# Kernel tuning notes

Measured on AMD Instinct MI355X. Metric: run time of the kernel, lower is better.

Reference implementation:

```python
import jax, jax.numpy as jnp
import numpy as np

NAT, NN = 10000, 32
RSN, THETAN, NEMB = 16, 8, 4
RC = 5.0
ZETA = 16.0
FEAT = RSN * NEMB + RSN * THETAN * NEMB  # 576
PI = 3.141592653589793


def setup_inputs() -> dict:
    key = jax.random.key(0)
    ks = jax.random.split(key, 12)
    positions = jax.random.normal(ks[0], (NAT, 3), dtype=jnp.float32) * 2.0
    species_encoder = jax.random.normal(ks[1], (NAT, NEMB), dtype=jnp.float32)
    theta_s = jax.random.uniform(ks[2], (THETAN,), dtype=jnp.float32) * PI
    kn_rad = jnp.ones((1,), dtype=jnp.float32)
    neighbor_idx = jax.random.randint(ks[3], (NAT, NN), 0, NAT, dtype=jnp.int32)
    W1 = jax.random.normal(ks[4], (FEAT, 64), dtype=jnp.float32) / np.sqrt(FEAT)
    b1 = jnp.zeros((64,), dtype=jnp.float32)
    W2 = jax.random.normal(ks[5], (64, 64), dtype=jnp.float32) / 8.0
    b2 = jnp.zeros((64,), dtype=jnp.float32)
    W3 = jax.random.normal(ks[6], (64, 1), dtype=jnp.float32) / 8.0
    b3 = jnp.zeros((1,), dtype=jnp.float32)
    return {"positions": positions, "species_encoder": species_encoder,
            "theta_s": theta_s, "kn_rad": kn_rad,
            "W1": W1, "b1": b1, "W2": W2, "b2": b2, "W3": W3, "b3": b3,
            "neighbor_idx": neighbor_idx}


def _bessel_radial(rnorm, kn_rad):
    # spherical-Bessel radial basis with smooth cosine cutoff (help_fn.bessel_function)
    fc = 0.5 * (jnp.cos(PI * rnorm / RC) + 1.0) * (rnorm < RC).astype(rnorm.dtype)
    k = jnp.arange(1, RSN + 1, dtype=rnorm.dtype)                     # [RSN]
    arg = (PI / RC) * kn_rad[0] * k[None, None, :] * rnorm[..., None]  # [nat,NN,RSN]
    return jnp.sqrt(2.0 / RC) * jnp.sin(arg) / rnorm[..., None] * fc[..., None]


def reference(positions, species_encoder, theta_s, kn_rad,
              W1, b1, W2, b2, W3, b3, neighbor_idx):
    # gather neighbor displacements: [nat, NN, 3]
    rij = positions[neighbor_idx] - positions[:, None, :]
    rnorm = jnp.linalg.norm(rij, axis=-1) + 1e-8                      # [nat, NN]

    bf = _bessel_radial(rnorm, kn_rad)                                # [nat, NN, RSN]
    # center-x-neighbor species embedding product (einsum 'ijk->ik->ijk')
    semb_ij = species_encoder[neighbor_idx] * species_encoder[:, None, :]  # [nat,NN,NEMB]

    # radial descriptors: [nat, RSN, NEMB] -> [nat, RSN*NEMB]
    desc_rad = jnp.einsum('ijl,ijm->ilm', bf, semb_ij).reshape(NAT, -1)

    # angular part
    rij_unit = rij / rnorm[..., None]
    cos_ijk = jnp.einsum('ijc,ikc->ijk', rij_unit, rij_unit)          # [nat,NN,NN]
    cos_ijk = jnp.clip(cos_ijk, -1.0 + 1e-6, 1.0 - 1e-6)
    sin_ijk = jnp.sqrt(1.0 - cos_ijk * cos_ijk)
    ct, st = jnp.cos(theta_s), jnp.sin(theta_s)

    # factorized per-bond channel tensor P: [nat, NN, RSN*NEMB]
    P = jnp.einsum('ijl,ijm->ijlm', bf, semb_ij).reshape(NAT, NN, RSN * NEMB)
    pref = 2.0 ** (1.0 - ZETA)
    ang = []
    for t in range(THETAN):  # small fixed loop over angle centers
        cosd = cos_ijk * ct[t] + sin_ijk * st[t]                      # cos(theta - theta_s)
        A = pref * (1.0 + cosd) ** ZETA                               # [nat,NN,NN]
        C = jnp.einsum('ijk,ijp->ikp', A, P)                          # contract over j
        ang.append(jnp.sum(C * P, axis=1))                            # [nat, RSN*NEMB]
    desc_ang = jnp.stack(ang, axis=1).reshape(NAT, -1)                # [nat, THETAN*RSN*NEMB]

    desc = jnp.concatenate([desc_rad, desc_ang], axis=1)              # [nat, FEAT]

    # per-atom MLP -> atomic energies, scatter-sum to total energy
    h = jnp.tanh(desc @ W1 + b1)
    h = jnp.tanh(h @ W2 + b2)
    e_atom = (h @ W3 + b3)[:, 0]                                      # [nat]
    return jnp.sum(e_atom)
```

## Files before the change

### kernel.cpp

```cpp
#include <hip/hip_runtime.h>
#include <hip/hip_bf16.h>

#define NATC 10000
#define NATP 10016
#define NNC 32
#define RSNC 16
#define THETANC 8
#define NEMBC 4
#define FEATC 576

typedef __attribute__((ext_vector_type(8))) short short8;
typedef __attribute__((ext_vector_type(4))) float f32x4;
typedef __attribute__((ext_vector_type(2))) float f32x2;

static __device__ __forceinline__ short f2bf(float x) {
    union { __hip_bfloat16 h; short s; } u;
    u.h = __float2bfloat16(x);
    return u.s;
}

__global__ __launch_bounds__(256) void prep_kernel(
    const float* __restrict__ W1, const float* __restrict__ W2,
    const float* __restrict__ b3,
    ushort* __restrict__ W1p, ushort* __restrict__ W2p,
    float* __restrict__ out)
{
    const int gid = blockIdx.x * 256 + threadIdx.x;
    if (gid == 0) out[0] = (float)NATC * b3[0];
    if (gid < 4608) {
        const int l = gid & 63, ntks = gid >> 6;
        const int nt = ntks & 3, ks = ntks >> 2;
        const int q = l >> 4, c = l & 15;
        ushort pk[8];
        #pragma unroll
        for (int jj = 0; jj < 8; ++jj)
            pk[jj] = (ushort)f2bf(W1[(ks * 32 + q * 8 + jj) * 64 + nt * 16 + c]);
        #pragma unroll
        for (int jj = 0; jj < 8; ++jj) W1p[gid * 8 + jj] = pk[jj];
    } else {
        const int g = gid - 4608;
        const int l = g & 63, ntks = g >> 6;
        const int nt = ntks & 3, ks = ntks >> 2;
        const int q = l >> 4, c = l & 15;
        ushort pk[8];
        #pragma unroll
        for (int jj = 0; jj < 8; ++jj)
            pk[jj] = (ushort)f2bf(W2[(ks * 32 + q * 8 + jj) * 64 + nt * 16 + c]);
        #pragma unroll
        for (int jj = 0; jj < 8; ++jj) W2p[g * 8 + jj] = pk[jj];
    }
}

__global__ __launch_bounds__(256, 7) void desc_kernel(
    const float* __restrict__ pos,
    const float* __restrict__ spe,
    const float* __restrict__ theta_s,
    const float* __restrict__ kn_rad,
    const int* __restrict__ nidx,
    ushort* __restrict__ descb)
{
    constexpr float RC = 5.0f;
    constexpr float PI_F = 3.14159265358979323846f;
    constexpr float SF = 0.52213689121f;

    __shared__ f32x4 Pt4[64 * 9];
    __shared__ f32x4 cs4[32 * 17];
    __shared__ float thc[16];
    __shared__ __attribute__((aligned(16))) char uni[4096];

    float* const Pt    = (float*)Pt4;
    float* const ux    = (float*)uni;
    float* const uy    = ux + 32;
    float* const uz    = ux + 64;
    float* const rbase = ux + 96;
    float* const rw    = ux + 128;
    float* const bfs   = ux + 160;
    float* const ses   = ux + 704;
    short* const Pb    = (short*)uni;

    const int i   = blockIdx.x;
    const int tid = threadIdx.x;

    if (tid < NNC) {
        const int j = tid;
        const int n = nidx[i * NNC + j];
        const float pix = pos[i * 3 + 0], piy = pos[i * 3 + 1], piz = pos[i * 3 + 2];
        const float dx = pos[n * 3 + 0] - pix;
        const float dy = pos[n * 3 + 1] - piy;
        const float dz = pos[n * 3 + 2] - piz;
        const float r = sqrtf(dx * dx + dy * dy + dz * dz) + 1e-8f;
        const float inv = 1.0f / r;
        ux[j] = dx * inv; uy[j] = dy * inv; uz[j] = dz * inv;
        const float fc = (r < RC) ? 0.5f * (cosf(PI_F * r * (1.0f / RC)) + 1.0f) : 0.0f;
        rbase[j] = sqrtf(2.0f / RC) * inv * fc;
        rw[j]    = (PI_F / RC) * kn_rad[0] * r;
        #pragma unroll
        for (int m = 0; m < NEMBC; ++m)
            ses[j * 5 + m] = spe[n * NEMBC + m] * spe[i * NEMBC + m];
    } else if (tid >= 64 && tid < 72) {
        const int t = tid - 64;
        const float th = theta_s[t];
        thc[2 * t]     = SF * cosf(th);
        thc[2 * t + 1] = SF * sinf(th);
    }
    __syncthreads();

    #pragma unroll
    for (int k = 0; k < 2; ++k) {
        const int e = tid + k * 256;
        const int j = e >> 4, l = e & 15;
        bfs[j * 17 + l] = rbase[j] * sinf(rw[j] * (float)(l + 1));
    }
    __syncthreads();

    #pragma unroll
    for (int k = 0; k < 8; ++k) {
        const int e = tid + k * 256;
        const int j = e & 31, p = e >> 5;
        Pt[p * 36 + j] = bfs[j * 17 + (p >> 2)] * ses[j * 5 + (p & 3)];
    }
    #pragma unroll
    for (int k = 0; k < 4; ++k) {
        const int e = tid + k * 256;
        const int kk = e & 31, j = e >> 5;
        float cv = ux[j] * ux[kk] + uy[j] * uy[kk] + uz[j] * uz[kk];
        cv = fminf(fmaxf(cv, -1.0f + 1e-6f), 1.0f - 1e-6f);
        f32x2 csv;
        csv[0] = cv;
        csv[1] = sqrtf(fmaxf(1.0f - cv * cv, 0.0f));
        ((f32x2*)cs4)[kk * 34 + j] = csv;
    }
    __syncthreads();

    {
        const int nt = tid >> 6, l2 = tid & 63;
        const int q2 = l2 >> 4, c2 = l2 & 15;
        const f32x4 x0 = Pt4[(nt * 16 + c2) * 9 + q2 * 2];
        const f32x4 x1 = Pt4[(nt * 16 + c2) * 9 + q2 * 2 + 1];
        short8 pk;
        pk[0] = f2bf(x0[0]); pk[1] = f2bf(x0[1]); pk[2] = f2bf(x0[2]); pk[3] = f2bf(x0[3]);
        pk[4] = f2bf(x1[0]); pk[5] = f2bf(x1[1]); pk[6] = f2bf(x1[2]); pk[7] = f2bf(x1[3]);
        *(short8*)&Pb[tid * 8] = pk;
    }
    if (tid < 64) {
        const f32x4* pr = &Pt4[tid * 9];
        float s = 0.0f;
        #pragma unroll
        for (int kb = 0; kb < 8; ++kb) {
            const f32x4 v = pr[kb];
            s += v[0]; s += v[1]; s += v[2]; s += v[3];
        }
        descb[(size_t)i * FEATC + tid] = (ushort)f2bf(s);
    }
    __syncthreads();

    const int w = tid >> 6, l = tid & 63;
    const int q = l >> 4, c = l & 15;

    #pragma unroll
    for (int tt = 0; tt < 2; ++tt) {
        const int t = w + tt * 4;
        const float tc = thc[2 * t], ts = thc[2 * t + 1];

        short8 afr[2];
        #pragma unroll
        for (int mt = 0; mt < 2; ++mt) {
            const int kk = mt * 16 + c;
            const f32x4* crow = &cs4[kk * 17 + q * 4];
            const f32x4 vv[4] = { crow[0], crow[1], crow[2], crow[3] };
            #pragma unroll
            for (int jj = 0; jj < 8; ++jj) {
                const float cv = vv[jj >> 1][(jj & 1) * 2];
                const float sv = vv[jj >> 1][(jj & 1) * 2 + 1];
                const float y  = fmaf(cv, tc, fmaf(sv, ts, SF));
                const float y2 = y * y, y4 = y2 * y2, y8 = y4 * y4;
                afr[mt][jj] = f2bf(y8 * y8);
            }
        }

        f32x4 acc[2][4];
        #pragma unroll
        for (int mt = 0; mt < 2; ++mt)
            #pragma unroll
            for (int nt = 0; nt < 4; ++nt)
                acc[mt][nt] = (f32x4){0.0f, 0.0f, 0.0f, 0.0f};

        #pragma unroll
        for (int nt = 0; nt < 4; ++nt) {
            const short8 bfr = *(const short8*)&Pb[(nt * 64 + l) * 8];
            acc[0][nt] = __builtin_amdgcn_mfma_f32_16x16x32_bf16(afr[0], bfr, acc[0][nt], 0, 0, 0);
            acc[1][nt] = __builtin_amdgcn_mfma_f32_16x16x32_bf16(afr[1], bfr, acc[1][nt], 0, 0, 0);
        }

        float ptv[4];
        #pragma unroll
        for (int nt = 0; nt < 4; ++nt) {
            float s = 0.0f;
            #pragma unroll
            for (int mt = 0; mt < 2; ++mt) {
                const f32x4 pv = Pt4[(nt * 16 + c) * 9 + mt * 4 + q];
                #pragma unroll
                for (int r = 0; r < 4; ++r)
                    s = fmaf(acc[mt][nt][r], pv[r], s);
            }
            s += __shfl_xor(s, 16, 64);
            s += __shfl_xor(s, 32, 64);
            ptv[nt] = s;
        }
        const float v = (q == 0) ? ptv[0] : (q == 1) ? ptv[1] : (q == 2) ? ptv[2] : ptv[3];
        descb[(size_t)i * FEATC + 64 + t * 64 + l] = (ushort)f2bf(v);
    }
}

__global__ __launch_bounds__(256) void mlp_kernel(
    const ushort* __restrict__ descb,
    const ushort* __restrict__ W1p, const float* __restrict__ b1,
    const ushort* __restrict__ W2p, const float* __restrict__ b2,
    const float* __restrict__ W3,
    float* __restrict__ out)
{
    __shared__ __attribute__((aligned(16))) ushort H1b[16 * 72];
    __shared__ float red[4];

    const int tid = threadIdx.x;
    const int w = tid >> 6, l = tid & 63;
    const int q = l >> 4, c = l & 15;
    const int a0 = blockIdx.x * 16;

    f32x4 acc = (f32x4){0.0f, 0.0f, 0.0f, 0.0f};

    #pragma unroll 6
    for (int ks = 0; ks < 18; ++ks) {
        const short8 b   = *(const short8*)&W1p[((ks * 4 + w) * 64 + l) * 8];
        const short8 afr = *(const short8*)&descb[(size_t)(a0 + c) * FEATC + ks * 32 + q * 8];
        acc = __builtin_amdgcn_mfma_f32_16x16x32_bf16(afr, b, acc, 0, 0, 0);
    }

    const float b1v = b1[w * 16 + c];
    #pragma unroll
    for (int r = 0; r < 4; ++r)
        H1b[(q * 4 + r) * 72 + w * 16 + c] = (ushort)f2bf(tanhf(acc[r] + b1v));
    __syncthreads();

    f32x4 acc2 = (f32x4){0.0f, 0.0f, 0.0f, 0.0f};
    #pragma unroll
    for (int ks = 0; ks < 2; ++ks) {
        const short8 b   = *(const short8*)&W2p[((ks * 4 + w) * 64 + l) * 8];
        const short8 afr = *(const short8*)&H1b[c * 72 + ks * 32 + q * 8];
        acc2 = __builtin_amdgcn_mfma_f32_16x16x32_bf16(afr, b, acc2, 0, 0, 0);
    }

    const float b2v = b2[w * 16 + c];
    const float w3v = W3[w * 16 + c];
    float s = 0.0f;
    #pragma unroll
    for (int r = 0; r < 4; ++r) {
        const int a = a0 + q * 4 + r;
        if (a < NATC) s += tanhf(acc2[r] + b2v) * w3v;
    }
    #pragma unroll
    for (int off = 1; off <= 32; off <<= 1)
        s += __shfl_xor(s, off, 64);
    if (l == 0) red[w] = s;
    __syncthreads();
    if (tid == 0)
        atomicAdd(out, red[0] + red[1] + red[2] + red[3]);
}

extern "C" void kernel_launch(void* const* d_in, const int* in_sizes, int n_in,
                              void* d_out, int out_size, void* d_ws, size_t ws_size,
                              hipStream_t stream)
{
    const float* pos   = (const float*)d_in[0];
    const float* spe   = (const float*)d_in[1];
    const float* theta = (const float*)d_in[2];
    const float* kn    = (const float*)d_in[3];
    const float* W1    = (const float*)d_in[4];
    const float* b1    = (const float*)d_in[5];
    const float* W2    = (const float*)d_in[6];
    const float* b2    = (const float*)d_in[7];
    const float* W3    = (const float*)d_in[8];
    const float* b3    = (const float*)d_in[9];
    const int*   nidx  = (const int*)d_in[10];
    float* out = (float*)d_out;

    ushort* descb = (ushort*)d_ws;
    ushort* W1p   = (ushort*)((char*)d_ws + (size_t)NATP * FEATC * 2);
    ushort* W2p   = W1p + 4608 * 8;

    prep_kernel<<<20, 256, 0, stream>>>(W1, W2, b3, W1p, W2p, out);
    desc_kernel<<<NATC, 256, 0, stream>>>(pos, spe, theta, kn, nidx, descb);
    mlp_kernel<<<(NATC + 15) / 16, 256, 0, stream>>>(descb, W1p, b1, W2p, b2, W3, out);
}
```

Baseline: 134.4 us.

## Merge prep into desc kernel, use sin recurrence and packed FP32 math

New measurement: 132.3 us. About the same (-1.5%).

```diff
diff --git a/kernel.cpp b/kernel.cpp
--- a/kernel.cpp
+++ b/kernel.cpp
@@ -19,67 +19,87 @@
     return u.s;
 }
 
-__global__ __launch_bounds__(256) void prep_kernel(
+static __device__ __forceinline__ f32x2 pk_fma(f32x2 a, f32x2 b, f32x2 c) {
+    f32x2 d;
+    asm("v_pk_fma_f32 %0, %1, %2, %3" : "=v"(d) : "v"(a), "v"(b), "v"(c));
+    return d;
+}
+static __device__ __forceinline__ f32x2 pk_mul(f32x2 a, f32x2 b) {
+    f32x2 d;
+    asm("v_pk_mul_f32 %0, %1, %2" : "=v"(d) : "v"(a), "v"(b));
+    return d;
+}
+static __device__ __forceinline__ int cvt_pk_bf16(float lo, float hi) {
+    int r;
+    asm("v_cvt_pk_bf16_f32 %0, %1, %2" : "=v"(r) : "v"(lo), "v"(hi));
+    return r;
+}
+
+static __device__ __forceinline__ int pow16_pair(f32x2 cv, f32x2 sv,
+                                                 f32x2 tcv, f32x2 tsv, f32x2 sfv) {
+    f32x2 y = pk_fma(cv, tcv, pk_fma(sv, tsv, sfv));
+    y = pk_mul(y, y);
+    y = pk_mul(y, y);
+    y = pk_mul(y, y);
+    y = pk_mul(y, y);
+    return cvt_pk_bf16(y[0], y[1]);
+}
+
+__global__ __launch_bounds__(256, 5) void desc_kernel(
+    const float* __restrict__ pos,
+    const float* __restrict__ spe,
+    const float* __restrict__ theta_s,
+    const float* __restrict__ kn_rad,
+    const int* __restrict__ nidx,
+    ushort* __restrict__ descb,
     const float* __restrict__ W1, const float* __restrict__ W2,
     const float* __restrict__ b3,
     ushort* __restrict__ W1p, ushort* __restrict__ W2p,
     float* __restrict__ out)
 {
-    const int gid = blockIdx.x * 256 + threadIdx.x;
-    if (gid == 0) out[0] = (float)NATC * b3[0];
-    if (gid < 4608) {
-        const int l = gid & 63, ntks = gid >> 6;
-        const int nt = ntks & 3, ks = ntks >> 2;
-        const int q = l >> 4, c = l & 15;
-        ushort pk[8];
-        #pragma unroll
-        for (int jj = 0; jj < 8; ++jj)
-            pk[jj] = (ushort)f2bf(W1[(ks * 32 + q * 8 + jj) * 64 + nt * 16 + c]);
-        #pragma unroll
-        for (int jj = 0; jj < 8; ++jj) W1p[gid * 8 + jj] = pk[jj];
-    } else {
-        const int g = gid - 4608;
-        const int l = g & 63, ntks = g >> 6;
-        const int nt = ntks & 3, ks = ntks >> 2;
-        const int q = l >> 4, c = l & 15;
-        ushort pk[8];
-        #pragma unroll
-        for (int jj = 0; jj < 8; ++jj)
-            pk[jj] = (ushort)f2bf(W2[(ks * 32 + q * 8 + jj) * 64 + nt * 16 + c]);
-        #pragma unroll
-        for (int jj = 0; jj < 8; ++jj) W2p[g * 8 + jj] = pk[jj];
-    }
-}
-
-__global__ __launch_bounds__(256, 7) void desc_kernel(
-    const float* __restrict__ pos,
-    const float* __restrict__ spe,
-    const float* __restrict__ theta_s,
-    const float* __restrict__ kn_rad,
-    const int* __restrict__ nidx,
-    ushort* __restrict__ descb)
-{
     constexpr float RC = 5.0f;
     constexpr float PI_F = 3.14159265358979323846f;
     constexpr float SF = 0.52213689121f;
 
-    __shared__ f32x4 Pt4[64 * 9];
-    __shared__ f32x4 cs4[32 * 17];
+    const int tid = threadIdx.x;
+
+    if (blockIdx.x >= NATC) {
+        const int gid = (blockIdx.x - NATC) * 256 + tid;
+        if (gid == 0) out[0] = (float)NATC * b3[0];
+        if (gid < 4608) {
+            const int l = gid & 63, ntks = gid >> 6;
+            const int nt = ntks & 3, ks = ntks >> 2;
+            const int qq = l >> 4, cc = l & 15;
+            ushort pk[8];
+            #pragma unroll
+            for (int jj = 0; jj < 8; ++jj)
+                pk[jj] = (ushort)f2bf(W1[(ks * 32 + qq * 8 + jj) * 64 + nt * 16 + cc]);
+            #pragma unroll
+            for (int jj = 0; jj < 8; ++jj) W1p[gid * 8 + jj] = pk[jj];
+        } else {
+            const int g = gid - 4608;
+            const int l = g & 63, ntks = g >> 6;
+            const int nt = ntks & 3, ks = ntks >> 2;
+            const int qq = l >> 4, cc = l & 15;
+            ushort pk[8];
+            #pragma unroll
+            for (int jj = 0; jj < 8; ++jj)
+                pk[jj] = (ushort)f2bf(W2[(ks * 32 + qq * 8 + jj) * 64 + nt * 16 + cc]);
+            #pragma unroll
+            for (int jj = 0; jj < 8; ++jj) W2p[g * 8 + jj] = pk[jj];
+        }
+        return;
+    }
+
+    __shared__ __attribute__((aligned(16))) float Pt[64 * 36];
+    __shared__ __attribute__((aligned(16))) float cosP[32 * 36];
+    __shared__ __attribute__((aligned(16))) float sinP[32 * 36];
     __shared__ float thc[16];
-    __shared__ __attribute__((aligned(16))) char uni[4096];
-
-    float* const Pt    = (float*)Pt4;
-    float* const ux    = (float*)uni;
-    float* const uy    = ux + 32;
-    float* const uz    = ux + 64;
-    float* const rbase = ux + 96;
-    float* const rw    = ux + 128;
-    float* const bfs   = ux + 160;
-    float* const ses   = ux + 704;
-    short* const Pb    = (short*)uni;
-
-    const int i   = blockIdx.x;
-    const int tid = threadIdx.x;
+    __shared__ float ux[32], uy[32], uz[32];
+    __shared__ __attribute__((aligned(16))) float ses[32 * 5];
+    __shared__ __attribute__((aligned(16))) float bfs[32 * 17];
+
+    const int i = blockIdx.x;
 
     if (tid < NNC) {
         const int j = tid;
@@ -92,8 +112,17 @@
         const float inv = 1.0f / r;
         ux[j] = dx * inv; uy[j] = dy * inv; uz[j] = dz * inv;
         const float fc = (r < RC) ? 0.5f * (cosf(PI_F * r * (1.0f / RC)) + 1.0f) : 0.0f;
-        rbase[j] = sqrtf(2.0f / RC) * inv * fc;
-        rw[j]    = (PI_F / RC) * kn_rad[0] * r;
+        const float rb = sqrtf(2.0f / RC) * inv * fc;
+        const float x  = (PI_F / RC) * kn_rad[0] * r;
+        float skm1 = sinf(x), skm2 = 0.0f;
+        const float c2x = 2.0f * cosf(x);
+        bfs[j * 17 + 0] = rb * skm1;
+        #pragma unroll
+        for (int k = 2; k <= 16; ++k) {
+            const float sk = fmaf(c2x, skm1, -skm2);
+            bfs[j * 17 + (k - 1)] = rb * sk;
+            skm2 = skm1; skm1 = sk;
+        }
         #pragma unroll
         for (int m = 0; m < NEMBC; ++m)
             ses[j * 5 + m] = spe[n * NEMBC + m] * spe[i * NEMBC + m];
@@ -106,14 +135,6 @@
     __syncthreads();
 
     #pragma unroll
-    for (int k = 0; k < 2; ++k) {
-        const int e = tid + k * 256;
-        const int j = e >> 4, l = e & 15;
-        bfs[j * 17 + l] = rbase[j] * sinf(rw[j] * (float)(l + 1));
-    }
-    __syncthreads();
-
-    #pragma unroll
     for (int k = 0; k < 8; ++k) {
         const int e = tid + k * 256;
         const int j = e & 31, p = e >> 5;
@@ -122,28 +143,16 @@
     #pragma unroll
     for (int k = 0; k < 4; ++k) {
         const int e = tid + k * 256;
-        const int kk = e & 31, j = e >> 5;
+        const int j = e & 31, kk = e >> 5;
         float cv = ux[j] * ux[kk] + uy[j] * uy[kk] + uz[j] * uz[kk];
         cv = fminf(fmaxf(cv, -1.0f + 1e-6f), 1.0f - 1e-6f);
-        f32x2 csv;
-        csv[0] = cv;
-        csv[1] = sqrtf(fmaxf(1.0f - cv * cv, 0.0f));
-        ((f32x2*)cs4)[kk * 34 + j] = csv;
+        cosP[kk * 36 + j] = cv;
+        sinP[kk * 36 + j] = sqrtf(fmaxf(1.0f - cv * cv, 0.0f));
     }
     __syncthreads();
 
-    {
-        const int nt = tid >> 6, l2 = tid & 63;
-        const int q2 = l2 >> 4, c2 = l2 & 15;
-        const f32x4 x0 = Pt4[(nt * 16 + c2) * 9 + q2 * 2];
-        const f32x4 x1 = Pt4[(nt * 16 + c2) * 9 + q2 * 2 + 1];
-        short8 pk;
-        pk[0] = f2bf(x0[0]); pk[1] = f2bf(x0[1]); pk[2] = f2bf(x0[2]); pk[3] = f2bf(x0[3]);
-        pk[4] = f2bf(x1[0]); pk[5] = f2bf(x1[1]); pk[6] = f2bf(x1[2]); pk[7] = f2bf(x1[3]);
-        *(short8*)&Pb[tid * 8] = pk;
-    }
     if (tid < 64) {
-        const f32x4* pr = &Pt4[tid * 9];
+        const f32x4* pr = (const f32x4*)&Pt[tid * 36];
         float s = 0.0f;
         #pragma unroll
         for (int kb = 0; kb < 8; ++kb) {
@@ -152,30 +161,43 @@
         }
         descb[(size_t)i * FEATC + tid] = (ushort)f2bf(s);
     }
-    __syncthreads();
 
     const int w = tid >> 6, l = tid & 63;
     const int q = l >> 4, c = l & 15;
+
+    short8 pbr[4];
+    #pragma unroll
+    for (int nt = 0; nt < 4; ++nt) {
+        const f32x4* prow = (const f32x4*)&Pt[(nt * 16 + c) * 36 + q * 8];
+        const f32x4 p0 = prow[0], p1 = prow[1];
+        union { short8 s8; int i4[4]; } u;
+        u.i4[0] = cvt_pk_bf16(p0[0], p0[1]);
+        u.i4[1] = cvt_pk_bf16(p0[2], p0[3]);
+        u.i4[2] = cvt_pk_bf16(p1[0], p1[1]);
+        u.i4[3] = cvt_pk_bf16(p1[2], p1[3]);
+        pbr[nt] = u.s8;
+    }
 
     #pragma unroll
     for (int tt = 0; tt < 2; ++tt) {
         const int t = w + tt * 4;
         const float tc = thc[2 * t], ts = thc[2 * t + 1];
+        const f32x2 tcv = {tc, tc}, tsv = {ts, ts}, sfv = {SF, SF};
 
         short8 afr[2];
         #pragma unroll
         for (int mt = 0; mt < 2; ++mt) {
             const int kk = mt * 16 + c;
-            const f32x4* crow = &cs4[kk * 17 + q * 4];
-            const f32x4 vv[4] = { crow[0], crow[1], crow[2], crow[3] };
-            #pragma unroll
-            for (int jj = 0; jj < 8; ++jj) {
-                const float cv = vv[jj >> 1][(jj & 1) * 2];
-                const float sv = vv[jj >> 1][(jj & 1) * 2 + 1];
-                const float y  = fmaf(cv, tc, fmaf(sv, ts, SF));
-                const float y2 = y * y, y4 = y2 * y2, y8 = y4 * y4;
-                afr[mt][jj] = f2bf(y8 * y8);
-            }
+            const f32x4* cr = (const f32x4*)&cosP[kk * 36 + q * 8];
+            const f32x4* sr = (const f32x4*)&sinP[kk * 36 + q * 8];
+            const f32x4 c0 = cr[0], c1 = cr[1];
+            const f32x4 s0 = sr[0], s1 = sr[1];
+            union { short8 s8; int i4[4]; } u;
+            u.i4[0] = pow16_pair((f32x2){c0[0], c0[1]}, (f32x2){s0[0], s0[1]}, tcv, tsv, sfv);
+            u.i4[1] = pow16_pair((f32x2){c0[2], c0[3]}, (f32x2){s0[2], s0[3]}, tcv, tsv, sfv);
+            u.i4[2] = pow16_pair((f32x2){c1[0], c1[1]}, (f32x2){s1[0], s1[1]}, tcv, tsv, sfv);
+            u.i4[3] = pow16_pair((f32x2){c1[2], c1[3]}, (f32x2){s1[2], s1[3]}, tcv, tsv, sfv);
+            afr[mt] = u.s8;
         }
 
         f32x4 acc[2][4];
@@ -187,22 +209,22 @@
 
         #pragma unroll
         for (int nt = 0; nt < 4; ++nt) {
-            const short8 bfr = *(const short8*)&Pb[(nt * 64 + l) * 8];
-            acc[0][nt] = __builtin_amdgcn_mfma_f32_16x16x32_bf16(afr[0], bfr, acc[0][nt], 0, 0, 0);
-            acc[1][nt] = __builtin_amdgcn_mfma_f32_16x16x32_bf16(afr[1], bfr, acc[1][nt], 0, 0, 0);
+            acc[0][nt] = __builtin_amdgcn_mfma_f32_16x16x32_bf16(afr[0], pbr[nt], acc[0][nt], 0, 0, 0);
+            acc[1][nt] = __builtin_amdgcn_mfma_f32_16x16x32_bf16(afr[1], pbr[nt], acc[1][nt], 0, 0, 0);
         }
 
         float ptv[4];
         #pragma unroll
         for (int nt = 0; nt < 4; ++nt) {
-            float s = 0.0f;
+            f32x2 s2 = {0.0f, 0.0f};
             #pragma unroll
             for (int mt = 0; mt < 2; ++mt) {
-                const f32x4 pv = Pt4[(nt * 16 + c) * 9 + mt * 4 + q];
-                #pragma unroll
-                for (int r = 0; r < 4; ++r)
-                    s = fmaf(acc[mt][nt][r], pv[r], s);
+                const f32x4 pv = *(const f32x4*)&Pt[(nt * 16 + c) * 36 + mt * 16 + q * 4];
+                const f32x4 av = acc[mt][nt];
+                s2 = pk_fma((f32x2){av[0], av[1]}, (f32x2){pv[0], pv[1]}, s2);
+                s2 = pk_fma((f32x2){av[2], av[3]}, (f32x2){pv[2], pv[3]}, s2);
             }
+            float s = s2[0] + s2[1];
             s += __shfl_xor(s, 16, 64);
             s += __shfl_xor(s, 32, 64);
             ptv[nt] = s;
@@ -288,7 +310,7 @@
     ushort* W1p   = (ushort*)((char*)d_ws + (size_t)NATP * FEATC * 2);
     ushort* W2p   = W1p + 4608 * 8;
 
-    prep_kernel<<<20, 256, 0, stream>>>(W1, W2, b3, W1p, W2p, out);
-    desc_kernel<<<NATC, 256, 0, stream>>>(pos, spe, theta, kn, nidx, descb);
+    desc_kernel<<<NATC + 20, 256, 0, stream>>>(pos, spe, theta, kn, nidx, descb,
+                                               W1, W2, b3, W1p, W2p, out);
     mlp_kernel<<<(NATC + 15) / 16, 256, 0, stream>>>(descb, W1p, b1, W2p, b2, W3, out);
 }
```
